# Performance work log

Hardware: AMD Instinct MI355X
Metric: run time of the kernel (lower is better)

The kernel has to match this reference:

```python
import jax, jax.numpy as jnp
import numpy as np

N_NODES = 100000
NEG_SLOPE = 0.2

def _glorot(key, shape):
    lim = float(np.sqrt(6.0 / (shape[0] + shape[-1])))
    return jax.random.uniform(key, shape, jnp.float32, -lim, lim)

def setup_inputs() -> dict:
    key = jax.random.key(0)
    ks = jax.random.split(key, 12)
    x = jax.random.normal(ks[0], (N_NODES, 128), jnp.float32)
    edge_index = jax.random.randint(ks[1], (2, 3200000), 0, N_NODES).astype(jnp.int64)
    # layer 1: in=128, heads=2, out=8
    W1 = _glorot(ks[2], (128, 16)); a_src1 = _glorot(ks[3], (2, 8)); a_dst1 = _glorot(ks[4], (2, 8)); b1 = jnp.zeros((16,), jnp.float32)
    # layer 2: in=16, heads=2, out=4
    W2 = _glorot(ks[5], (16, 8)); a_src2 = _glorot(ks[6], (2, 4)); a_dst2 = _glorot(ks[7], (2, 4)); b2 = jnp.zeros((8,), jnp.float32)
    # layer 3: in=8, heads=1, out=4
    W3 = _glorot(ks[8], (8, 4)); a_src3 = _glorot(ks[9], (1, 4)); a_dst3 = _glorot(ks[10], (1, 4)); b3 = jnp.zeros((4,), jnp.float32)
    Wc = _glorot(ks[11], (4, 2)); bc = jnp.zeros((2,), jnp.float32)
    return {"x": x, "edge_index": edge_index,
            "W1": W1, "a_src1": a_src1, "a_dst1": a_dst1, "b1": b1,
            "W2": W2, "a_src2": a_src2, "a_dst2": a_dst2, "b2": b2,
            "W3": W3, "a_src3": a_src3, "a_dst3": a_dst3, "b3": b3,
            "Wc": Wc, "bc": bc}

def gat_layer(x, src, dst, W, a_src, a_dst, b, H, C):
    # PyG GATConv: linear -> per-node attention terms -> per-edge leaky_relu -> segment softmax over dst -> scatter-sum
    N = x.shape[0]
    h = (x @ W).reshape(N, H, C)                         # [N,H,C]
    alpha_s = jnp.sum(h * a_src, axis=-1)                # [N,H]
    alpha_d = jnp.sum(h * a_dst, axis=-1)                # [N,H]
    e = jax.nn.leaky_relu(alpha_s[src] + alpha_d[dst], NEG_SLOPE)  # [E,H]
    m = jax.ops.segment_max(e, dst, num_segments=N)      # [N,H]
    ex = jnp.exp(e - m[dst])
    denom = jax.ops.segment_sum(ex, dst, num_segments=N)
    alpha = ex / (denom[dst] + 1e-16)                    # [E,H]
    out = jax.ops.segment_sum(h[src] * alpha[:, :, None], dst, num_segments=N)  # [N,H,C]
    return out.reshape(N, H * C) + b

def reference(x, edge_index, W1, a_src1, a_dst1, b1, W2, a_src2, a_dst2, b2, W3, a_src3, a_dst3, b3, Wc, bc):
    N = x.shape[0]
    loop = jnp.arange(N, dtype=edge_index.dtype)
    src = jnp.concatenate([edge_index[0], loop])  # add_self_loops=True (PyG default)
    dst = jnp.concatenate([edge_index[1], loop])
    h = jax.nn.relu(gat_layer(x, src, dst, W1, a_src1, a_dst1, b1, 2, 8))
    h = jax.nn.relu(gat_layer(h, src, dst, W2, a_src2, a_dst2, b2, 2, 4))
    # dropout p=0.5 is identity in eval mode
    h = gat_layer(h, src, dst, W3, a_src3, a_dst3, b3, 1, 4)
    return h @ Wc + bc
```

## Files before the change

### kernel.cpp

```cpp
#include <hip/hip_runtime.h>

#define TB 256
#define NGRP 8
#define NB_P 1024
#define TBP 256
#define NBKT 256
#define SORT_T 1024
#define STG_CAP 13312
#define STG2_CAP 3200
#define RCAP 4

typedef int      i4v __attribute__((ext_vector_type(4)));
typedef float    f4v __attribute__((ext_vector_type(4)));
typedef _Float16 h4v __attribute__((ext_vector_type(4)));
typedef _Float16 h8v __attribute__((ext_vector_type(8)));

struct __align__(16) Rec2 { _Float16 h[8]; float as[2]; float pad[2]; };
struct __align__(16) Rec3 { _Float16 h[4]; float as; float pad; };

static __device__ __forceinline__ float leaky(float x) {
  return x > 0.f ? x : 0.2f * x;
}


__global__ void __launch_bounds__(TB)
k_scatter_node1(const int* __restrict__ srcA, const int* __restrict__ dstA,
                int* __restrict__ cnt, int* __restrict__ loffG,
                int* __restrict__ epkPriv, int E4, int E, unsigned M, int R,
                int CH4, int CHP,
                const float* __restrict__ xin, const float* __restrict__ W1,
                const float* __restrict__ a_src, const float* __restrict__ a_dst,
                _Float16* __restrict__ hout, float* __restrict__ ad_, int N) {
  __shared__ __align__(16) char smem[18960];
  const int t = threadIdx.x;
  if (blockIdx.x < NB_P) {
    const int kblk = blockIdx.x;
    int* lc   = (int*)smem;
    int* loff = (int*)(smem + 4096);
    int* lcur = (int*)(smem + 5136);
    int* stg  = (int*)(smem + 6160);
    for (int i = t; i < 4 * NBKT; i += TBP) lc[i] = 0;
    __syncthreads();
    int* lcw = lc + (t >> 6) * NBKT;
    const int bstart = kblk * CH4;
    const int bend = min(E4, bstart + CH4);
    const i4v* d4 = reinterpret_cast<const i4v*>(dstA);
    const i4v* s4 = reinterpret_cast<const i4v*>(srcA);
    i4v dr[RCAP], sr[RCAP];
    int it1 = 0;
    for (int i = bstart + t; i < bend; i += TBP, ++it1) {
      i4v d = __builtin_nontemporal_load(&d4[i]);
      i4v sv = __builtin_nontemporal_load(&s4[i]);
      if (it1 < RCAP) { dr[it1] = d; sr[it1] = sv; }
#pragma unroll
      for (int k = 0; k < 4; ++k) atomicAdd(&lcw[__umulhi((unsigned)d[k], M)], 1);
    }
    if (kblk == NB_P - 1) {
      for (int i = E4 * 4 + t; i < E; i += TBP)
        atomicAdd(&lcw[__umulhi((unsigned)dstA[i], M)], 1);
    }
    __syncthreads();
    int c = 0;
    if (t < NBKT) {
      c = lc[t] + lc[NBKT + t] + lc[2 * NBKT + t] + lc[3 * NBKT + t];
      loff[t] = c;
    }
    __syncthreads();
    for (int o = 1; o < NBKT; o <<= 1) {
      int u = (t < NBKT && t >= o) ? loff[t - o] : 0;
      __syncthreads();
      if (t < NBKT) loff[t] += u;
      __syncthreads();
    }
    if (t < NBKT) {
      int excl = loff[t] - c;
      cnt[t * NB_P + kblk] = c;
      loffG[kblk * NBKT + t] = excl;
      lcur[t] = excl;
      loff[t] = excl;
      if (t == NBKT - 1) loff[NBKT] = excl + c;
    }
    __syncthreads();
    int it2 = 0;
    for (int i = bstart + t; i < bend; i += TBP, ++it2) {
      i4v d = (it2 < RCAP) ? dr[it2] : d4[i];
      i4v sv = (it2 < RCAP) ? sr[it2] : s4[i];
#pragma unroll
      for (int k = 0; k < 4; ++k) {
        int dd = d[k];
        int b = __umulhi((unsigned)dd, M);
        int pos = atomicAdd(&lcur[b], 1);
        stg[pos] = ((dd - b * R) << 17) | sv[k];
      }
    }
    if (kblk == NB_P - 1) {
      for (int i = E4 * 4 + t; i < E; i += TBP) {
        int dd = dstA[i];
        int b = __umulhi((unsigned)dd, M);
        int pos = atomicAdd(&lcur[b], 1);
        stg[pos] = ((dd - b * R) << 17) | srcA[i];
      }
    }
    __syncthreads();
    const int total = loff[NBKT];
    int* dst = epkPriv + (size_t)kblk * CHP;
    for (int i = t; i < total; i += TBP) dst[i] = stg[i];
  } else {
    constexpr int IN = 128, OUT = 16, SPLIT = 4, NPB = TB / SPLIT, PIN4 = IN / SPLIT / 4;
    float* Ws = (float*)smem;
    float* Ad = (float*)(smem + 8192);
    const int bid = blockIdx.x - NB_P;
    for (int i = t; i < IN * OUT; i += TB) Ws[i] = W1[i];
    if (t < OUT) Ad[t] = a_dst[t];
    __syncthreads();
    const int j = t & (SPLIT - 1);
    const int n = bid * NPB + t / SPLIT;
    if (n >= N) return;
    float acc[OUT];
#pragma unroll
    for (int q = 0; q < OUT; ++q) acc[q] = 0.f;
    const f4v* x4 = reinterpret_cast<const f4v*>(xin + (size_t)n * IN + j * (IN / SPLIT));
#pragma unroll
    for (int k4 = 0; k4 < PIN4; ++k4) {
      f4v xv = __builtin_nontemporal_load(&x4[k4]);
      const int kb = j * (IN / SPLIT) + 4 * k4;
#pragma unroll
      for (int q = 0; q < OUT; ++q) {
        acc[q] += xv[0] * Ws[(kb + 0) * OUT + q];
        acc[q] += xv[1] * Ws[(kb + 1) * OUT + q];
        acc[q] += xv[2] * Ws[(kb + 2) * OUT + q];
        acc[q] += xv[3] * Ws[(kb + 3) * OUT + q];
      }
    }
#pragma unroll
    for (int o = 1; o < SPLIT; o <<= 1) {
#pragma unroll
      for (int q = 0; q < OUT; ++q) acc[q] += __shfl_xor(acc[q], o);
    }
    if (j < OUT / 4) {
      h4v v;
      v[0] = (_Float16)acc[4 * j + 0];
      v[1] = (_Float16)acc[4 * j + 1];
      v[2] = (_Float16)acc[4 * j + 2];
      v[3] = (_Float16)acc[4 * j + 3];
      reinterpret_cast<h4v*>(hout + (size_t)n * OUT)[j] = v;
    }
    if (j < 2) {
      float dd = 0.f;
#pragma unroll
      for (int c = 0; c < 8; ++c) dd += acc[j * 8 + c] * Ad[j * 8 + c];
      ad_[n * 2 + j] = dd;
    }
  }
}

__global__ void k_bscan1(const int* __restrict__ cnt, int* __restrict__ off,
                         int* __restrict__ colTotal) {
  __shared__ int sh[NB_P];
  const int t = threadIdx.x;
  const int b = blockIdx.x;
  int v = cnt[b * NB_P + t];
  sh[t] = v;
  __syncthreads();
  for (int o = 1; o < NB_P; o <<= 1) {
    int u = (t >= o) ? sh[t - o] : 0;
    __syncthreads();
    sh[t] += u;
    __syncthreads();
  }
  off[b * NB_P + t] = sh[t] - v;
  if (t == NB_P - 1) colTotal[b] = sh[t];
}

__global__ void k_bscan2(const int* __restrict__ colTotal, int* __restrict__ bucketBase) {
  __shared__ int sh[NBKT];
  const int t = threadIdx.x;
  int v = colTotal[t];
  sh[t] = v;
  __syncthreads();
  for (int o = 1; o < NBKT; o <<= 1) {
    int u = (t >= o) ? sh[t - o] : 0;
    __syncthreads();
    sh[t] += u;
    __syncthreads();
  }
  bucketBase[t] = sh[t] - v;
  if (t == NBKT - 1) bucketBase[NBKT] = sh[t];
}

__global__ void k_bsort(const int* __restrict__ epkPriv, const int* __restrict__ off,
                        const int* __restrict__ loffG, const int* __restrict__ bucketBase,
                        int* __restrict__ rowStart, int* __restrict__ colIdx,
                        int N, int R, int E, int CHP) {
  __shared__ int offRow[NB_P];
  __shared__ int loffCol[NB_P];
  __shared__ int sc[512];
  __shared__ int stg[STG_CAP];
  const int b = (blockIdx.x & (NGRP - 1)) * (NBKT / NGRP) + (blockIdx.x >> 3);
  const int lo = bucketBase[b], hi = bucketBase[b + 1];
  const int cntB = hi - lo;
  const int nodeLo = b * R;
  const int nN = min(R, N - nodeLo);
  const int t = threadIdx.x;
  for (int i = t; i < NB_P; i += SORT_T) {
    offRow[i] = off[b * NB_P + i];
    loffCol[i] = loffG[i * NBKT + b];
  }
  if (t < 512) sc[t] = 0;
  __syncthreads();
  auto fetch = [&](int i) -> int {
    int loQ = 0, hiQ = NB_P;
#pragma unroll
    for (int it = 0; it < 10; ++it) {
      int mid = (loQ + hiQ) >> 1;
      if (offRow[mid] <= i) loQ = mid; else hiQ = mid;
    }
    return epkPriv[(size_t)loQ * CHP + loffCol[loQ] + (i - offRow[loQ])];
  };
  for (int i = t; i < cntB; i += SORT_T) {
    int pk = fetch(i);
    atomicAdd(&sc[pk >> 17], 1);
  }
  __syncthreads();
  int own = (t < 512) ? sc[t] : 0;
  for (int o = 1; o < 512; o <<= 1) {
    int u = (t < 512 && t >= o) ? sc[t - o] : 0;
    __syncthreads();
    if (t < 512) sc[t] += u;
    __syncthreads();
  }
  if (t < nN) rowStart[nodeLo + t] = lo + sc[t] - own;
  if (b == NBKT - 1 && t == 0) rowStart[N] = E;
  if (t < 512) sc[t] -= own;
  __syncthreads();
  if (cntB <= STG_CAP) {
    for (int i = t; i < cntB; i += SORT_T) {
      int pk = fetch(i);
      int pos = atomicAdd(&sc[pk >> 17], 1);
      stg[pos] = pk & 0x1FFFF;
    }
    __syncthreads();
    for (int i = t; i < cntB; i += SORT_T) colIdx[lo + i] = stg[i];
  } else {
    for (int i = t; i < cntB; i += SORT_T) {
      int pk = fetch(i);
      int pos = lo + atomicAdd(&sc[pk >> 17], 1);
      colIdx[pos] = pk & 0x1FFFF;
    }
  }
}


__global__ void k_edge12(const int* __restrict__ rowStart, const int* __restrict__ colIdx,
                         const _Float16* __restrict__ h1, const float* __restrict__ as1w,
                         const float* __restrict__ ad_, const float* __restrict__ b1,
                         const float* __restrict__ W2, const float* __restrict__ as2w,
                         const float* __restrict__ ad2w, Rec2* __restrict__ r2,
                         float* __restrict__ ad2, int N, int R8) {
  constexpr int L = 2, S = 4, LS = 8, NPB = TB / LS;
  __shared__ float Ws2[128], A1s[16], A2s[8], A2d[8], B1s[16];
  if (threadIdx.x < 128) Ws2[threadIdx.x] = W2[threadIdx.x];
  if (threadIdx.x < 16) {
    A1s[threadIdx.x] = as1w[threadIdx.x];
    B1s[threadIdx.x] = b1[threadIdx.x];
  }
  if (threadIdx.x < 8) {
    A2s[threadIdx.x] = as2w[threadIdx.x];
    A2d[threadIdx.x] = ad2w[threadIdx.x];
  }
  __syncthreads();
  const int g = blockIdx.x & (NGRP - 1);
  const int lb = blockIdx.x / NGRP;
  const int lane = threadIdx.x % LS;
  const int sub = lane >> 1;
  const int j = lane & 1;
  const int n = g * R8 + lb * NPB + threadIdx.x / LS;
  const int nEnd = min((g + 1) * R8, N);
  if (n >= nEnd) return;
  const float adv = ad_[n * 2 + j];
  float aw[8];
#pragma unroll
  for (int c = 0; c < 8; ++c) aw[c] = A1s[j * 8 + c];
  const int start = rowStart[n];
  const int end = rowStart[n + 1];
  float s = 0.f, acc[8];
#pragma unroll
  for (int q = 0; q < 8; ++q) acc[q] = 0.f;
  if (sub == 0) {
    h8v a0 = reinterpret_cast<const h8v*>(h1 + (size_t)n * 16)[j];
    float e = 0.f;
#pragma unroll
    for (int c = 0; c < 8; ++c) e += (float)a0[c] * aw[c];
    float p = __expf(leaky(e + adv));
    s = p;
#pragma unroll
    for (int q = 0; q < 8; ++q) acc[q] = p * (float)a0[q];
  }
  const int base = start & ~3;
  const int nch = (end - base + 3) >> 2;
  i4v cv;
  if (sub < nch) cv = *reinterpret_cast<const i4v*>(colIdx + base + 4 * sub);
  for (int t = sub; t < nch; t += S) {
    i4v nxt = cv;
    if (t + S < nch) nxt = *reinterpret_cast<const i4v*>(colIdx + base + 4 * (t + S));
    const int i0 = base + 4 * t;
#pragma unroll
    for (int k = 0; k < 4; ++k) {
      const bool ok = (i0 + k >= start) && (i0 + k < end);
      const int src = ok ? cv[k] : n;
      h8v hv = reinterpret_cast<const h8v*>(h1 + (size_t)src * 16)[j];
      float e = 0.f;
#pragma unroll
      for (int c = 0; c < 8; ++c) e += (float)hv[c] * aw[c];
      float p = ok ? __expf(leaky(e + adv)) : 0.f;
      s += p;
#pragma unroll
      for (int q = 0; q < 8; ++q) acc[q] += p * (float)hv[q];
    }
    cv = nxt;
  }
#pragma unroll
  for (int off = L; off < LS; off <<= 1) {
    s += __shfl_xor(s, off);
#pragma unroll
    for (int q = 0; q < 8; ++q) acc[q] += __shfl_xor(acc[q], off);
  }
  if (sub == 0) {
    float inv = 1.f / (s + 1e-16f);
    float o1v[8];
#pragma unroll
    for (int q = 0; q < 8; ++q) o1v[q] = fmaxf(acc[q] * inv + B1s[j * 8 + q], 0.f);
    float h2p[8];
#pragma unroll
    for (int q = 0; q < 8; ++q) {
      float tacc = 0.f;
#pragma unroll
      for (int c = 0; c < 8; ++c) tacc += o1v[c] * Ws2[(j * 8 + c) * 8 + q];
      h2p[q] = tacc;
    }
    float h2f[8];
#pragma unroll
    for (int q = 0; q < 8; ++q) h2f[q] = h2p[q] + __shfl_xor(h2p[q], 1);
    h4v v;
#pragma unroll
    for (int q = 0; q < 4; ++q) v[q] = (_Float16)h2f[j * 4 + q];
    reinterpret_cast<h4v*>(r2[n].h)[j] = v;
    float ss = 0.f, dd = 0.f;
#pragma unroll
    for (int c = 0; c < 4; ++c) {
      ss += h2f[j * 4 + c] * A2s[j * 4 + c];
      dd += h2f[j * 4 + c] * A2d[j * 4 + c];
    }
    r2[n].as[j] = ss;
    ad2[n * 2 + j] = dd;
  }
}


__global__ void k_edge23(const int* __restrict__ rowStart, const int* __restrict__ colIdx,
                         const Rec2* __restrict__ r2, const float* __restrict__ ad_,
                         const float* __restrict__ b2, const float* __restrict__ W3,
                         const float* __restrict__ as3w, const float* __restrict__ ad3w,
                         Rec3* __restrict__ r3, float* __restrict__ ad3, int N, int R8) {
  constexpr int L = 2, S = 4, LS = 8, NPB = TB / LS;
  __shared__ float Ws3[32], A3s[4], A3d[4], B2s[8];
  if (threadIdx.x < 32) Ws3[threadIdx.x] = W3[threadIdx.x];
  if (threadIdx.x < 4) {
    A3s[threadIdx.x] = as3w[threadIdx.x];
    A3d[threadIdx.x] = ad3w[threadIdx.x];
  }
  if (threadIdx.x < 8) B2s[threadIdx.x] = b2[threadIdx.x];
  __syncthreads();
  const int g = blockIdx.x & (NGRP - 1);
  const int lb = blockIdx.x / NGRP;
  const int lane = threadIdx.x % LS;
  const int sub = lane >> 1;
  const int j = lane & 1;
  const int n = g * R8 + lb * NPB + threadIdx.x / LS;
  const int nEnd = min((g + 1) * R8, N);
  if (n >= nEnd) return;
  const float adv = ad_[n * 2 + j];
  const int start = rowStart[n];
  const int end = rowStart[n + 1];
  float s = 0.f, acc[4];
#pragma unroll
  for (int q = 0; q < 4; ++q) acc[q] = 0.f;
  if (sub == 0) {
    float p = __expf(leaky(r2[n].as[j] + adv));
    h4v a0 = reinterpret_cast<const h4v*>(r2[n].h)[j];
    s = p;
#pragma unroll
    for (int q = 0; q < 4; ++q) acc[q] = p * (float)a0[q];
  }
  const int base = start & ~3;
  const int nch = (end - base + 3) >> 2;
  i4v cv;
  if (sub < nch) cv = *reinterpret_cast<const i4v*>(colIdx + base + 4 * sub);
  for (int t = sub; t < nch; t += S) {
    i4v nxt = cv;
    if (t + S < nch) nxt = *reinterpret_cast<const i4v*>(colIdx + base + 4 * (t + S));
    const int i0 = base + 4 * t;
#pragma unroll
    for (int k = 0; k < 4; ++k) {
      const bool ok = (i0 + k >= start) && (i0 + k < end);
      const int src = ok ? cv[k] : n;
      h4v hv = reinterpret_cast<const h4v*>(r2[src].h)[j];
      float e = r2[src].as[j];
      float p = ok ? __expf(leaky(e + adv)) : 0.f;
      s += p;
#pragma unroll
      for (int q = 0; q < 4; ++q) acc[q] += p * (float)hv[q];
    }
    cv = nxt;
  }
#pragma unroll
  for (int off = L; off < LS; off <<= 1) {
    s += __shfl_xor(s, off);
#pragma unroll
    for (int q = 0; q < 4; ++q) acc[q] += __shfl_xor(acc[q], off);
  }
  if (sub == 0) {
    float inv = 1.f / (s + 1e-16f);
    float o2v[4];
#pragma unroll
    for (int q = 0; q < 4; ++q) o2v[q] = fmaxf(acc[q] * inv + B2s[j * 4 + q], 0.f);
    float h3p[4];
#pragma unroll
    for (int q = 0; q < 4; ++q) {
      float tacc = 0.f;
#pragma unroll
      for (int c = 0; c < 4; ++c) tacc += o2v[c] * Ws3[(j * 4 + c) * 4 + q];
      h3p[q] = tacc;
    }
    float h3f[4];
#pragma unroll
    for (int q = 0; q < 4; ++q) h3f[q] = h3p[q] + __shfl_xor(h3p[q], 1);
    if (j == 0) {
      Rec3 rec;
#pragma unroll
      for (int q = 0; q < 4; ++q) rec.h[q] = (_Float16)h3f[q];
      float ss = 0.f, dd = 0.f;
#pragma unroll
      for (int c = 0; c < 4; ++c) {
        ss += h3f[c] * A3s[c];
        dd += h3f[c] * A3d[c];
      }
      rec.as = ss;
      rec.pad = 0.f;
      r3[n] = rec;
      ad3[n] = dd;
    }
  }
}


__global__ void k_edge3(const int* __restrict__ rowStart, const int* __restrict__ colIdx,
                        const Rec3* __restrict__ r3, const float* __restrict__ ad_,
                        const float* __restrict__ b3, const float* __restrict__ Wc,
                        const float* __restrict__ bc, float* __restrict__ out,
                        int N, int R8) {
  constexpr int S = 8;
  constexpr int NPB = TB / S;
  const int g = blockIdx.x & (NGRP - 1);
  const int lb = blockIdx.x / NGRP;
  const int sub = threadIdx.x % S;
  const int n = g * R8 + lb * NPB + threadIdx.x / S;
  const int nEnd = min((g + 1) * R8, N);
  if (n >= nEnd) return;
  const float adv = ad_[n];
  const int start = rowStart[n];
  const int end = rowStart[n + 1];
  float s = 0.f, acc0 = 0.f, acc1 = 0.f, acc2 = 0.f, acc3 = 0.f;
  if (sub == 0) {
    Rec3 rec = r3[n];
    float p = __expf(leaky(rec.as + adv));
    s = p;
    acc0 = p * (float)rec.h[0];
    acc1 = p * (float)rec.h[1];
    acc2 = p * (float)rec.h[2];
    acc3 = p * (float)rec.h[3];
  }
  const int base = start & ~3;
  const int nch = (end - base + 3) >> 2;
  i4v cv;
  if (sub < nch) cv = *reinterpret_cast<const i4v*>(colIdx + base + 4 * sub);
  for (int t = sub; t < nch; t += S) {
    i4v nxt = cv;
    if (t + S < nch) nxt = *reinterpret_cast<const i4v*>(colIdx + base + 4 * (t + S));
    const int i0 = base + 4 * t;
#pragma unroll
    for (int k = 0; k < 4; ++k) {
      const bool ok = (i0 + k >= start) && (i0 + k < end);
      const int src = ok ? cv[k] : n;
      Rec3 rec = r3[src];
      float p = ok ? __expf(leaky(rec.as + adv)) : 0.f;
      s += p;
      acc0 += p * (float)rec.h[0];
      acc1 += p * (float)rec.h[1];
      acc2 += p * (float)rec.h[2];
      acc3 += p * (float)rec.h[3];
    }
    cv = nxt;
  }
#pragma unroll
  for (int off = 1; off < S; off <<= 1) {
    s += __shfl_xor(s, off);
    acc0 += __shfl_xor(acc0, off);
    acc1 += __shfl_xor(acc1, off);
    acc2 += __shfl_xor(acc2, off);
    acc3 += __shfl_xor(acc3, off);
  }
  if (sub == 0) {
    float inv = 1.f / (s + 1e-16f);
    float o0 = acc0 * inv + b3[0];
    float o1 = acc1 * inv + b3[1];
    float o2 = acc2 * inv + b3[2];
    float o3 = acc3 * inv + b3[3];
    float2 r;
    r.x = o0 * Wc[0] + o1 * Wc[2] + o2 * Wc[4] + o3 * Wc[6] + bc[0];
    r.y = o0 * Wc[1] + o1 * Wc[3] + o2 * Wc[5] + o3 * Wc[7] + bc[1];
    reinterpret_cast<float2*>(out)[n] = r;
  }
}


extern "C" void kernel_launch(void* const* d_in, const int* in_sizes, int n_in,
                              void* d_out, int out_size, void* d_ws, size_t ws_size,
                              hipStream_t stream) {
  const float* x    = (const float*)d_in[0];
  const int*   ei   = (const int*)d_in[1];
  const float* W1   = (const float*)d_in[2];
  const float* as1w = (const float*)d_in[3];
  const float* ad1w = (const float*)d_in[4];
  const float* b1   = (const float*)d_in[5];
  const float* W2   = (const float*)d_in[6];
  const float* as2w = (const float*)d_in[7];
  const float* ad2w = (const float*)d_in[8];
  const float* b2   = (const float*)d_in[9];
  const float* W3   = (const float*)d_in[10];
  const float* as3w = (const float*)d_in[11];
  const float* ad3w = (const float*)d_in[12];
  const float* b3   = (const float*)d_in[13];
  const float* Wc   = (const float*)d_in[14];
  const float* bc   = (const float*)d_in[15];
  float* out = (float*)d_out;

  const int N = in_sizes[0] / 128;
  const int E = in_sizes[1] / 2;
  const int* srcA = ei;
  const int* dstA = ei + E;

  char* p = (char*)d_ws;
  auto alloc = [&](size_t bytes) -> void* {
    void* r = (void*)p;
    p += (bytes + 255) & ~(size_t)255;
    return r;
  };
  const int E4  = E >> 2;
  const int CH4 = (E4 + NB_P - 1) / NB_P;
  const int CHP = CH4 * 4 + 8;

  int* cnt        = (int*)alloc((size_t)NBKT * NB_P * 4);
  int* off        = (int*)alloc((size_t)NBKT * NB_P * 4);
  int* loffG      = (int*)alloc((size_t)NB_P * NBKT * 4);
  int* colTotal   = (int*)alloc(NBKT * 4);
  int* bucketBase = (int*)alloc((NBKT + 1) * 4);
  int* rowStart   = (int*)alloc((size_t)(N + 1) * 4);
  int* epkPriv    = (int*)alloc((size_t)NB_P * CHP * 4);
  int* colIdx     = (int*)alloc((size_t)E * 4 + 256);
  _Float16* h1 = (_Float16*)alloc((size_t)N * 16 * 2);
  float* ad1 = (float*)alloc((size_t)N * 2 * 4);
  Rec2* r2   = (Rec2*)alloc((size_t)N * sizeof(Rec2));
  float* ad2 = (float*)alloc((size_t)N * 2 * 4);
  Rec3* r3   = (Rec3*)alloc((size_t)N * sizeof(Rec3));
  float* ad3 = (float*)alloc((size_t)N * 4);

  const int R   = (N + NBKT - 1) / NBKT;
  const unsigned M = (unsigned)(((1ULL << 32) + R - 1) / R);
  const int R8  = R * (NBKT / NGRP);

  const int nb1 = (N + (TB / 4) - 1) / (TB / 4);
  const int ge8 = NGRP * ((R8 + (TB / 8) - 1) / (TB / 8));

  k_scatter_node1<<<NB_P + nb1, TB, 0, stream>>>(srcA, dstA, cnt, loffG, epkPriv,
                                                 E4, E, M, R, CH4, CHP,
                                                 x, W1, as1w, ad1w, h1, ad1, N);
  k_bscan1<<<NBKT, NB_P, 0, stream>>>(cnt, off, colTotal);
  k_bscan2<<<1, NBKT, 0, stream>>>(colTotal, bucketBase);
  k_bsort<<<NBKT, SORT_T, 0, stream>>>(epkPriv, off, loffG, bucketBase, rowStart,
                                       colIdx, N, R, E, CHP);

  k_edge12<<<ge8, TB, 0, stream>>>(rowStart, colIdx, h1, as1w, ad1, b1, W2, as2w, ad2w,
                                   r2, ad2, N, R8);
  k_edge23<<<ge8, TB, 0, stream>>>(rowStart, colIdx, r2, ad2, b2, W3, as3w, ad3w,
                                   r3, ad3, N, R8);
  k_edge3<<<ge8, TB, 0, stream>>>(rowStart, colIdx, r3, ad3, b3, Wc, bc, out, N, R8);
}
```

Measured before the change: 160.9 us.

## Software-pipeline neighbor gathers in GAT aggregation and interleave scatter/node blocks

In the three per-layer aggregation kernels, the neighbor feature gathers for the next chunk of edges are now issued one iteration ahead, and column indices two iterations ahead, so gather latency overlaps with the exp/accumulate math of the current chunk. The fused scatter/node1 kernel also interleaves scatter blocks and layer-1 projection blocks (even/odd block ids) so both kinds of work are spread across the device instead of running in two separate phases. The prefetching raises register pressure and may lower occupancy. The interleaving changes which block ids run concurrently.

```diff
diff --git a/kernel.cpp b/kernel.cpp
--- a/kernel.cpp
+++ b/kernel.cpp
@@ -33,8 +33,10 @@
                 _Float16* __restrict__ hout, float* __restrict__ ad_, int N) {
   __shared__ __align__(16) char smem[18960];
   const int t = threadIdx.x;
-  if (blockIdx.x < NB_P) {
-    const int kblk = blockIdx.x;
+  const int bid = blockIdx.x;
+  const bool isScatter = (bid < 2 * NB_P) && ((bid & 1) == 0);
+  if (isScatter) {
+    const int kblk = bid >> 1;
     int* lc   = (int*)smem;
     int* loff = (int*)(smem + 4096);
     int* lcur = (int*)(smem + 5136);
@@ -106,15 +108,15 @@
     int* dst = epkPriv + (size_t)kblk * CHP;
     for (int i = t; i < total; i += TBP) dst[i] = stg[i];
   } else {
+    const int nodeBid = (bid < 2 * NB_P) ? (bid >> 1) : (NB_P + (bid - 2 * NB_P));
     constexpr int IN = 128, OUT = 16, SPLIT = 4, NPB = TB / SPLIT, PIN4 = IN / SPLIT / 4;
     float* Ws = (float*)smem;
     float* Ad = (float*)(smem + 8192);
-    const int bid = blockIdx.x - NB_P;
     for (int i = t; i < IN * OUT; i += TB) Ws[i] = W1[i];
     if (t < OUT) Ad[t] = a_dst[t];
     __syncthreads();
     const int j = t & (SPLIT - 1);
-    const int n = bid * NPB + t / SPLIT;
+    const int n = nodeBid * NPB + t / SPLIT;
     if (n >= N) return;
     float acc[OUT];
 #pragma unroll
@@ -296,19 +298,38 @@
 #pragma unroll
     for (int q = 0; q < 8; ++q) acc[q] = p * (float)a0[q];
   }
+  const h8v* hrows = reinterpret_cast<const h8v*>(h1);
   const int base = start & ~3;
   const int nch = (end - base + 3) >> 2;
-  i4v cv;
-  if (sub < nch) cv = *reinterpret_cast<const i4v*>(colIdx + base + 4 * sub);
-  for (int t = sub; t < nch; t += S) {
-    i4v nxt = cv;
-    if (t + S < nch) nxt = *reinterpret_cast<const i4v*>(colIdx + base + 4 * (t + S));
-    const int i0 = base + 4 * t;
+  const int nmine = (nch > sub) ? ((nch - sub + S - 1) / S) : 0;
+  int ti = sub;
+  i4v cv0, cv1;
+  h8v g0, g1, g2, g3;
+  if (nmine >= 1) cv0 = *reinterpret_cast<const i4v*>(colIdx + base + 4 * sub);
+  if (nmine >= 2) cv1 = *reinterpret_cast<const i4v*>(colIdx + base + 4 * (sub + S));
+  if (nmine >= 1) {
+    const int i0 = base + 4 * ti;
+    g0 = hrows[(size_t)(((i0 + 0 >= start) && (i0 + 0 < end)) ? cv0[0] : n) * 2 + j];
+    g1 = hrows[(size_t)(((i0 + 1 >= start) && (i0 + 1 < end)) ? cv0[1] : n) * 2 + j];
+    g2 = hrows[(size_t)(((i0 + 2 >= start) && (i0 + 2 < end)) ? cv0[2] : n) * 2 + j];
+    g3 = hrows[(size_t)(((i0 + 3 >= start) && (i0 + 3 < end)) ? cv0[3] : n) * 2 + j];
+  }
+  for (int m = 0; m < nmine; ++m) {
+    const int i0 = base + 4 * ti;
+    i4v cv2 = cv1;
+    if (m + 2 < nmine) cv2 = *reinterpret_cast<const i4v*>(colIdx + base + 4 * (ti + 2 * S));
+    h8v n0 = g0, n1 = g1, n2 = g2, n3 = g3;
+    if (m + 1 < nmine) {
+      const int ni0 = base + 4 * (ti + S);
+      n0 = hrows[(size_t)(((ni0 + 0 >= start) && (ni0 + 0 < end)) ? cv1[0] : n) * 2 + j];
+      n1 = hrows[(size_t)(((ni0 + 1 >= start) && (ni0 + 1 < end)) ? cv1[1] : n) * 2 + j];
+      n2 = hrows[(size_t)(((ni0 + 2 >= start) && (ni0 + 2 < end)) ? cv1[2] : n) * 2 + j];
+      n3 = hrows[(size_t)(((ni0 + 3 >= start) && (ni0 + 3 < end)) ? cv1[3] : n) * 2 + j];
+    }
 #pragma unroll
     for (int k = 0; k < 4; ++k) {
       const bool ok = (i0 + k >= start) && (i0 + k < end);
-      const int src = ok ? cv[k] : n;
-      h8v hv = reinterpret_cast<const h8v*>(h1 + (size_t)src * 16)[j];
+      h8v hv = (k == 0) ? g0 : (k == 1) ? g1 : (k == 2) ? g2 : g3;
       float e = 0.f;
 #pragma unroll
       for (int c = 0; c < 8; ++c) e += (float)hv[c] * aw[c];
@@ -317,7 +338,9 @@
 #pragma unroll
       for (int q = 0; q < 8; ++q) acc[q] += p * (float)hv[q];
     }
-    cv = nxt;
+    cv0 = cv1; cv1 = cv2;
+    g0 = n0; g1 = n1; g2 = n2; g3 = n3;
+    ti += S;
   }
 #pragma unroll
   for (int off = L; off < LS; off <<= 1) {
@@ -394,24 +417,46 @@
   }
   const int base = start & ~3;
   const int nch = (end - base + 3) >> 2;
-  i4v cv;
-  if (sub < nch) cv = *reinterpret_cast<const i4v*>(colIdx + base + 4 * sub);
-  for (int t = sub; t < nch; t += S) {
-    i4v nxt = cv;
-    if (t + S < nch) nxt = *reinterpret_cast<const i4v*>(colIdx + base + 4 * (t + S));
-    const int i0 = base + 4 * t;
+  const int nmine = (nch > sub) ? ((nch - sub + S - 1) / S) : 0;
+  int ti = sub;
+  i4v cv0, cv1;
+  h4v g0, g1, g2, g3;
+  float e0, e1, e2, e3;
+  auto issue = [&](const i4v& cv, int i0, h4v& o0, h4v& o1, h4v& o2, h4v& o3,
+                   float& f0, float& f1, float& f2, float& f3) {
+    int s0 = ((i0 + 0 >= start) && (i0 + 0 < end)) ? cv[0] : n;
+    int s1 = ((i0 + 1 >= start) && (i0 + 1 < end)) ? cv[1] : n;
+    int s2 = ((i0 + 2 >= start) && (i0 + 2 < end)) ? cv[2] : n;
+    int s3 = ((i0 + 3 >= start) && (i0 + 3 < end)) ? cv[3] : n;
+    o0 = reinterpret_cast<const h4v*>(r2[s0].h)[j]; f0 = r2[s0].as[j];
+    o1 = reinterpret_cast<const h4v*>(r2[s1].h)[j]; f1 = r2[s1].as[j];
+    o2 = reinterpret_cast<const h4v*>(r2[s2].h)[j]; f2 = r2[s2].as[j];
+    o3 = reinterpret_cast<const h4v*>(r2[s3].h)[j]; f3 = r2[s3].as[j];
+  };
+  if (nmine >= 1) cv0 = *reinterpret_cast<const i4v*>(colIdx + base + 4 * sub);
+  if (nmine >= 2) cv1 = *reinterpret_cast<const i4v*>(colIdx + base + 4 * (sub + S));
+  if (nmine >= 1) issue(cv0, base + 4 * ti, g0, g1, g2, g3, e0, e1, e2, e3);
+  for (int m = 0; m < nmine; ++m) {
+    const int i0 = base + 4 * ti;
+    i4v cv2 = cv1;
+    if (m + 2 < nmine) cv2 = *reinterpret_cast<const i4v*>(colIdx + base + 4 * (ti + 2 * S));
+    h4v n0 = g0, n1 = g1, n2 = g2, n3 = g3;
+    float f0 = e0, f1 = e1, f2 = e2, f3 = e3;
+    if (m + 1 < nmine) issue(cv1, base + 4 * (ti + S), n0, n1, n2, n3, f0, f1, f2, f3);
 #pragma unroll
     for (int k = 0; k < 4; ++k) {
       const bool ok = (i0 + k >= start) && (i0 + k < end);
-      const int src = ok ? cv[k] : n;
-      h4v hv = reinterpret_cast<const h4v*>(r2[src].h)[j];
-      float e = r2[src].as[j];
+      h4v hv = (k == 0) ? g0 : (k == 1) ? g1 : (k == 2) ? g2 : g3;
+      float e = (k == 0) ? e0 : (k == 1) ? e1 : (k == 2) ? e2 : e3;
       float p = ok ? __expf(leaky(e + adv)) : 0.f;
       s += p;
 #pragma unroll
       for (int q = 0; q < 4; ++q) acc[q] += p * (float)hv[q];
     }
-    cv = nxt;
+    cv0 = cv1; cv1 = cv2;
+    g0 = n0; g1 = n1; g2 = n2; g3 = n3;
+    e0 = f0; e1 = f1; e2 = f2; e3 = f3;
+    ti += S;
   }
 #pragma unroll
   for (int off = L; off < LS; off <<= 1) {
@@ -482,17 +527,29 @@
   }
   const int base = start & ~3;
   const int nch = (end - base + 3) >> 2;
-  i4v cv;
-  if (sub < nch) cv = *reinterpret_cast<const i4v*>(colIdx + base + 4 * sub);
-  for (int t = sub; t < nch; t += S) {
-    i4v nxt = cv;
-    if (t + S < nch) nxt = *reinterpret_cast<const i4v*>(colIdx + base + 4 * (t + S));
-    const int i0 = base + 4 * t;
+  const int nmine = (nch > sub) ? ((nch - sub + S - 1) / S) : 0;
+  int ti = sub;
+  i4v cv0, cv1;
+  Rec3 g0, g1, g2, g3;
+  auto issue = [&](const i4v& cv, int i0, Rec3& o0, Rec3& o1, Rec3& o2, Rec3& o3) {
+    o0 = r3[((i0 + 0 >= start) && (i0 + 0 < end)) ? cv[0] : n];
+    o1 = r3[((i0 + 1 >= start) && (i0 + 1 < end)) ? cv[1] : n];
+    o2 = r3[((i0 + 2 >= start) && (i0 + 2 < end)) ? cv[2] : n];
+    o3 = r3[((i0 + 3 >= start) && (i0 + 3 < end)) ? cv[3] : n];
+  };
+  if (nmine >= 1) cv0 = *reinterpret_cast<const i4v*>(colIdx + base + 4 * sub);
+  if (nmine >= 2) cv1 = *reinterpret_cast<const i4v*>(colIdx + base + 4 * (sub + S));
+  if (nmine >= 1) issue(cv0, base + 4 * ti, g0, g1, g2, g3);
+  for (int m = 0; m < nmine; ++m) {
+    const int i0 = base + 4 * ti;
+    i4v cv2 = cv1;
+    if (m + 2 < nmine) cv2 = *reinterpret_cast<const i4v*>(colIdx + base + 4 * (ti + 2 * S));
+    Rec3 n0 = g0, n1 = g1, n2 = g2, n3 = g3;
+    if (m + 1 < nmine) issue(cv1, base + 4 * (ti + S), n0, n1, n2, n3);
 #pragma unroll
     for (int k = 0; k < 4; ++k) {
       const bool ok = (i0 + k >= start) && (i0 + k < end);
-      const int src = ok ? cv[k] : n;
-      Rec3 rec = r3[src];
+      Rec3 rec = (k == 0) ? g0 : (k == 1) ? g1 : (k == 2) ? g2 : g3;
       float p = ok ? __expf(leaky(rec.as + adv)) : 0.f;
       s += p;
       acc0 += p * (float)rec.h[0];
@@ -500,7 +557,9 @@
       acc2 += p * (float)rec.h[2];
       acc3 += p * (float)rec.h[3];
     }
-    cv = nxt;
+    cv0 = cv1; cv1 = cv2;
+    g0 = n0; g1 = n1; g2 = n2; g3 = n3;
+    ti += S;
   }
 #pragma unroll
   for (int off = 1; off < S; off <<= 1) {
```

Result: no change. 164.0 us (+1.9%).
